# Kernel tuning notes

Measured on AMD Instinct MI355X. Metric: run time of the kernel, lower is better.

## Reference

```python
import jax, jax.numpy as jnp
import numpy as np


def setup_inputs() -> dict:
    key = jax.random.key(0)
    kx, ke = jax.random.split(key)
    N, T, D, M = 64, 400, 1024, 256
    x = jax.random.normal(kx, (N, T, D), dtype=jnp.float32)
    embedding = jax.random.normal(ke, (M, D), dtype=jnp.float32)
    return {"x": x, "embedding": embedding}


def reference(x, embedding):
    # x: (N, T, D); embedding (codebook): (M, D)
    M, D = embedding.shape
    # L2_distance: normalize codebook rows, distances to detached x
    emb_norm = embedding / (jnp.linalg.norm(embedding, axis=1, keepdims=True) + 1e-4)
    x_flat = jax.lax.stop_gradient(x).reshape(-1, D)  # (N*T, D)
    distances = (jnp.sum(emb_norm ** 2, axis=1)[None, :]
                 + jnp.sum(x_flat ** 2, axis=1, keepdims=True)
                 - 2.0 * (x_flat @ emb_norm.T))  # (N*T, M)
    indices = jnp.argmin(distances, axis=-1)  # (N*T,)
    encodings = jax.nn.one_hot(indices, M, dtype=jnp.float32)  # (N*T, M)
    quantized = embedding[indices].reshape(x.shape)  # gather from UNnormalized codebook

    # commitment loss (both sides detached in original -> constant)
    commitment_loss = jnp.mean(
        (jax.lax.stop_gradient(x) - jax.lax.stop_gradient(quantized)) ** 2)

    # straight-through + average with quantized
    quantized_st = x + jax.lax.stop_gradient(quantized - x)
    quantized_ = (quantized_st + quantized) / 2.0

    avg_probs = jnp.mean(encodings, axis=0)  # (M,)
    perplexity = jnp.exp(-jnp.sum(avg_probs * jnp.log(avg_probs + 1e-10)))
    return quantized_, commitment_loss, perplexity
```

## Files before the change

### kernel.cpp

```cpp
#include <hip/hip_runtime.h>
#include <cstdint>
#include <cstddef>


typedef __attribute__((ext_vector_type(8))) short short8;
typedef __attribute__((ext_vector_type(4))) float f32x4;

namespace {
constexpr int kNT = 25600;
constexpr int kD  = 1024;
constexpr int kM  = 256;
constexpr size_t kQElems = (size_t)kNT * kD;

constexpr int WS_IMG_H = 0;
constexpr int WS_IMG_L = 131072;
constexpr int WS_E2N   = 262144;
constexpr int WS_SCL   = WS_E2N + kM;
constexpr int WS_E2R   = WS_SCL + kM;
constexpr int WS_COM   = WS_E2R + kM;
constexpr int WS_HIST  = WS_COM + 4;
constexpr int WS_TICKET = WS_HIST + kM;
}

typedef __attribute__((address_space(3))) unsigned int        lds_u32;
typedef const __attribute__((address_space(1))) unsigned int  glb_u32;
typedef const __attribute__((address_space(3))) char          lds_chc;

__device__ __forceinline__ void gl2lds16(const void* g, void* l) {
  __builtin_amdgcn_global_load_lds((glb_u32*)g, (lds_u32*)l, 16, 0, 0);
}

template <int OFF>
__device__ __forceinline__ short8 ldsr(lds_chc* p) {
  static_assert(OFF >= 0 && OFF < 65536, "ds offset immediate");
  short8 r;
  asm volatile("ds_read_b128 %0, %1 offset:%c2" : "=v"(r) : "v"(p), "i"(OFF));
  return r;
}
template <int OFF>
__device__ __forceinline__ void ldsw(lds_chc* p, short8 v) {
  static_assert(OFF >= 0 && OFF < 65536, "ds offset immediate");
  asm volatile("ds_write_b128 %0, %1 offset:%c2" :: "v"(p), "v"(v), "i"(OFF) : "memory");
}
__device__ __forceinline__ f32x4 gld4(const float* p) {
  f32x4 r;
  asm volatile("global_load_dwordx4 %0, %1, off" : "=v"(r) : "v"(p));
  return r;
}

__global__ __launch_bounds__(256) void vq_normalize(const float* __restrict__ emb,
                                                    float* __restrict__ ws) {
  const int m = blockIdx.x;
  const int t = threadIdx.x;

  if (t == 0) ((int*)(ws + WS_HIST))[m] = 0;
  if (m == 0 && t < 4) ws[WS_COM + t] = 0.0f;
  if (m == 0 && t == 4) ((int*)(ws + WS_TICKET))[0] = 0;

  const float4 v = reinterpret_cast<const float4*>(emb + (size_t)m * kD)[t];
  float s = v.x * v.x + v.y * v.y + v.z * v.z + v.w * v.w;
#pragma unroll
  for (int mask = 32; mask >= 1; mask >>= 1) s += __shfl_xor(s, mask);
  __shared__ float red[4];
  if ((t & 63) == 0) red[t >> 6] = s;
  __syncthreads();
  const float tot = red[0] + red[1] + red[2] + red[3];
  const float sc  = sqrtf(tot) + 1e-4f;
  const float inv = 1.0f / sc;
  const float4 nv = make_float4(v.x * inv, v.y * inv, v.z * inv, v.w * inv);

  float s2 = nv.x * nv.x + nv.y * nv.y + nv.z * nv.z + nv.w * nv.w;
#pragma unroll
  for (int mask = 32; mask >= 1; mask >>= 1) s2 += __shfl_xor(s2, mask);
  __syncthreads();
  if ((t & 63) == 0) red[t >> 6] = s2;
  __syncthreads();
  if (t == 0) {
    ws[WS_E2N + m] = red[0] + red[1] + red[2] + red[3];
    ws[WS_SCL + m] = sc;
    ws[WS_E2R + m] = tot;
  }

  unsigned short* imgh = (unsigned short*)(ws + WS_IMG_H);
  unsigned short* imgl = (unsigned short*)(ws + WS_IMG_L);
  const int c  = t >> 3;
  const int g  = (t >> 1) & 3;
  const int sq = g ^ ((m >> 1) & 3);
  const int base = c * 8192 + m * 32 + sq * 8 + 4 * (t & 1);
  ushort4 hq, lq;
#pragma unroll
  for (int j = 0; j < 4; ++j) {
    const float fv = (&nv.x)[j];
    const unsigned int b = __float_as_uint(fv);
    const unsigned short hi = (unsigned short)(b >> 16);
    const float lof = fv - __uint_as_float(b & 0xFFFF0000u);
    const unsigned short lo = (unsigned short)(__float_as_uint(lof) >> 16);
    (&hq.x)[j] = hi; (&lq.x)[j] = lo;
  }
  *(ushort4*)(imgh + base) = hq;
  *(ushort4*)(imgl + base) = lq;
}


struct Frags {
  short8 a0h, a1h, a2h, a3h, a0l, a1l, a2l, a3l;
  short8 b0h, b1h, b2h, b3h, b0l, b1l, b2l, b3l;
};

#define DMASTAGE(KCN)                                                          \
  {                                                                            \
    const unsigned short* gh_ = imgH + ((size_t)(KCN) << 13) + (w << 11) + (l << 3); \
    const unsigned short* gl_ = imgL + ((size_t)(KCN) << 13) + (w << 11) + (l << 3); \
    char* dg_ = pool + 16384 + w * 8192;                                       \
    gl2lds16(gh_,        dg_);                                                 \
    gl2lds16(gh_ +  512, dg_ + 1024);                                          \
    gl2lds16(gh_ + 1024, dg_ + 2048);                                          \
    gl2lds16(gh_ + 1536, dg_ + 3072);                                          \
    gl2lds16(gl_,        dg_ + 4096);                                          \
    gl2lds16(gl_ +  512, dg_ + 5120);                                          \
    gl2lds16(gl_ + 1024, dg_ + 6144);                                          \
    gl2lds16(gl_ + 1536, dg_ + 7168);                                          \
  }

#define PREFETCH9(PN, FN)                                                      \
  (FN).b0h = ldsr<16384 + 0 * 1024>(pB);                                       \
  (FN).b1h = ldsr<16384 + 1 * 1024>(pB);                                       \
  (FN).b2h = ldsr<16384 + 2 * 1024>(pB);                                       \
  (FN).b3h = ldsr<16384 + 3 * 1024>(pB);                                       \
  (FN).b0l = ldsr<16384 + 4096 + 0 * 1024>(pB);                                \
  (FN).b1l = ldsr<16384 + 4096 + 1 * 1024>(pB);                                \
  (FN).b2l = ldsr<16384 + 4096 + 2 * 1024>(pB);                                \
  (FN).b3l = ldsr<16384 + 4096 + 3 * 1024>(pB);                                \
  (FN).a0h = ldsr<(PN) * 8192 + 0 * 1024>(pA);                                 \
  (FN).a1h = ldsr<(PN) * 8192 + 1 * 1024>(pA);                                 \
  (FN).a2h = ldsr<(PN) * 8192 + 2 * 1024>(pA);                                 \
  (FN).a3h = ldsr<(PN) * 8192 + 3 * 1024>(pA);                                 \
  (FN).a0l = ldsr<(PN) * 8192 + 4096 + 0 * 1024>(pA);                          \
  (FN).a1l = ldsr<(PN) * 8192 + 4096 + 1 * 1024>(pA);                          \
  (FN).a2l = ldsr<(PN) * 8192 + 4096 + 2 * 1024>(pA);                          \
  (FN).a3l = ldsr<(PN) * 8192 + 4096 + 3 * 1024>(pA);

#define CONV8(F0, F1, AH, AL, X2EN)                                            \
  {                                                                            \
    union { short8 v; unsigned short u[8]; } H_, L_;                           \
    _Pragma("unroll")                                                          \
    for (int jj_ = 0; jj_ < 8; ++jj_) {                                        \
      const float fv_ = (jj_ < 4) ? (F0)[jj_] : (F1)[jj_ - 4];                 \
      const unsigned int b_ = __float_as_uint(fv_);                            \
      H_.u[jj_] = (unsigned short)(b_ >> 16);                                  \
      const float lo_ = fv_ - __uint_as_float(b_ & 0xFFFF0000u);               \
      L_.u[jj_] = (unsigned short)(__float_as_uint(lo_) >> 16);                \
      if (X2EN) x2 += fv_ * fv_;                                               \
    }                                                                          \
    AH = H_.v; AL = L_.v;                                                      \
  }

#define MMQ(AR, B0, B1, B2, B3, RT)                                                        \
  acc[RT][0] = __builtin_amdgcn_mfma_f32_16x16x32_bf16(AR, B0, acc[RT][0], 0, 0, 0);       \
  acc[RT][1] = __builtin_amdgcn_mfma_f32_16x16x32_bf16(AR, B1, acc[RT][1], 0, 0, 0);       \
  acc[RT][2] = __builtin_amdgcn_mfma_f32_16x16x32_bf16(AR, B2, acc[RT][2], 0, 0, 0);       \
  acc[RT][3] = __builtin_amdgcn_mfma_f32_16x16x32_bf16(AR, B3, acc[RT][3], 0, 0, 0);
#define MMPASS(A0, A1, A2, A3, B0, B1, B2, B3)                                 \
  MMQ(A0, B0, B1, B2, B3, 0) MMQ(A1, B0, B1, B2, B3, 1)                        \
  MMQ(A2, B0, B1, B2, B3, 2) MMQ(A3, B0, B1, B2, B3, 3)

#define VQ_ITER9(KC, P, FC, FN, XC0, XC1, XN0, XN1)                            \
  {                                                                            \
    __builtin_amdgcn_s_setprio(1);                                             \
    MMPASS(FC.a0h, FC.a1h, FC.a2h, FC.a3h, FC.b0h, FC.b1h, FC.b2h, FC.b3h)     \
    __builtin_amdgcn_s_setprio(0);                                             \
    asm volatile("s_waitcnt vmcnt(8)" ::: "memory");       \
    __builtin_amdgcn_sched_barrier(0);                                         \
    if ((KC) < 30) {                                                           \
      short8 cah, cal;                                                         \
      CONV8(XC0, XC1, cah, cal, 1)                                             \
      ldsw<(P) * 8192 + 0>(pW, cah);                                           \
      ldsw<(P) * 8192 + 4096>(pW, cal);                                        \
    }                                                                          \
    {                                                                          \
      const int kx_ = ((KC) + 3 < 32) ? (KC) + 3 : 31;                         \
      XN0 = gld4(xrow + kx_ * 32);                                             \
      XN1 = gld4(xrow + kx_ * 32 + 4);                                         \
    }                                                                          \
    asm volatile("s_waitcnt vmcnt(2)" ::: "memory");       \
    __builtin_amdgcn_sched_barrier(0);                                         \
    PREFETCH9((P) ^ 1, FN)                                    \
    __builtin_amdgcn_s_setprio(1);                                             \
    MMPASS(FC.a0h, FC.a1h, FC.a2h, FC.a3h, FC.b0l, FC.b1l, FC.b2l, FC.b3l)     \
    __builtin_amdgcn_s_setprio(0);                                             \
    asm volatile("s_waitcnt lgkmcnt(0)" ::: "memory");  \
    __builtin_amdgcn_sched_barrier(0);                                         \
    {                                                                          \
      const int kb_ = ((KC) + 2 < 32) ? (KC) + 2 : 31;                         \
      DMASTAGE(kb_)                                     \
    }                                                                          \
    __builtin_amdgcn_s_setprio(1);                                             \
    MMPASS(FC.a0l, FC.a1l, FC.a2l, FC.a3l, FC.b0h, FC.b1h, FC.b2h, FC.b3h)     \
    __builtin_amdgcn_s_setprio(0);                                             \
    __builtin_amdgcn_sched_barrier(0);                                         \
    __builtin_amdgcn_s_barrier();                            \
  }

__global__ __launch_bounds__(256, 2) void vq_main(const float* __restrict__ x,
                                                  const float* __restrict__ emb,
                                                  const float* __restrict__ wsc,
                                                  float* __restrict__ out,
                                                  float* __restrict__ commit_sum,
                                                  int* __restrict__ hist,
                                                  int* __restrict__ ticket) {
  __shared__ char pool[49152];

  const int t   = threadIdx.x;
  const int l   = t & 63;
  const int w   = t >> 6;
  const int nlo = l & 15;
  const int kq  = l >> 4;
  const int blk0 = blockIdx.x * 64;

  const unsigned short* imgH = (const unsigned short*)(wsc + WS_IMG_H);
  const unsigned short* imgL = (const unsigned short*)(wsc + WS_IMG_L);

  const float* xrow = x + (size_t)(blk0 + w * 16 + nlo) * kD + kq * 8;

  const int sqz = kq ^ ((nlo >> 1) & 3);
  lds_chc* base = (lds_chc*)pool;
  lds_chc* pA = base + nlo * 64 + sqz * 16;
  lds_chc* pB = base + w * 8192 + nlo * 64 + sqz * 16;
  lds_chc* pW = pA + w * 1024;

  f32x4 acc[4][4];
#pragma unroll
  for (int i = 0; i < 4; ++i)
#pragma unroll
    for (int j = 0; j < 4; ++j) acc[i][j] = (f32x4)0.0f;
  float x2 = 0.0f;

  Frags F0, F1;

  f32x4 xa0 = gld4(xrow);
  f32x4 xa1 = gld4(xrow + 4);
  f32x4 xb0 = gld4(xrow + 32);
  f32x4 xb1 = gld4(xrow + 36);
  DMASTAGE(0)
  asm volatile("s_waitcnt vmcnt(10)" ::: "memory");
  __builtin_amdgcn_sched_barrier(0);
  {
    short8 cah, cal;
    CONV8(xa0, xa1, cah, cal, 1)
    ldsw<0>(pW, cah);
    ldsw<4096>(pW, cal);
  }
  asm volatile("s_waitcnt vmcnt(8)" ::: "memory");
  __builtin_amdgcn_sched_barrier(0);
  {
    short8 cah, cal;
    CONV8(xb0, xb1, cah, cal, 1)
    ldsw<8192 + 0>(pW, cah);
    ldsw<8192 + 4096>(pW, cal);
  }
  xa0 = gld4(xrow + 2 * 32);
  xa1 = gld4(xrow + 2 * 32 + 4);
  asm volatile("s_waitcnt vmcnt(2)" ::: "memory");
  __builtin_amdgcn_sched_barrier(0);
  asm volatile("s_waitcnt lgkmcnt(0)" ::: "memory");
  __builtin_amdgcn_sched_barrier(0);
  __builtin_amdgcn_s_barrier();
  PREFETCH9(0, F0)
  asm volatile("s_waitcnt lgkmcnt(0)" ::: "memory");
  __builtin_amdgcn_sched_barrier(0);
  DMASTAGE(1)
  __builtin_amdgcn_s_barrier();

#pragma unroll 1
  for (int kk = 0; kk < 32; kk += 2) {
    VQ_ITER9(kk,     0, F0, F1, xa0, xa1, xb0, xb1)
    VQ_ITER9(kk + 1, 1, F1, F0, xb0, xb1, xa0, xa1)
  }

  asm volatile("s_waitcnt vmcnt(0)"
               :: "v"(xa0), "v"(xa1), "v"(xb0), "v"(xb1) : "memory");

  float* x2s  = (float*)pool;
  float* bvp  = x2s + 64;
  int*   bjp  = (int*)(bvp + 256);
  int*   idxs = bjp + 256;

  x2 += __shfl_xor(x2, 16);
  x2 += __shfl_xor(x2, 32);
  if (l < 16) x2s[w * 16 + l] = x2;

  float eN[4];
#pragma unroll
  for (int ct = 0; ct < 4; ++ct) eN[ct] = wsc[WS_E2N + w * 64 + ct * 16 + nlo];

  float bv[4][4]; int bj[4][4];
#pragma unroll
  for (int rt = 0; rt < 4; ++rt)
#pragma unroll
    for (int rg = 0; rg < 4; ++rg) { bv[rt][rg] = 3.0e38f; bj[rt][rg] = 0; }
#pragma unroll
  for (int ct = 0; ct < 4; ++ct) {
    const int j = w * 64 + ct * 16 + nlo;
#pragma unroll
    for (int rt = 0; rt < 4; ++rt)
#pragma unroll
      for (int rg = 0; rg < 4; ++rg) {
        const float v = eN[ct] - 2.0f * acc[rt][ct][rg];
        if (v < bv[rt][rg] || (v == bv[rt][rg] && j < bj[rt][rg])) {
          bv[rt][rg] = v; bj[rt][rg] = j;
        }
      }
  }
#pragma unroll
  for (int mk = 1; mk <= 8; mk <<= 1) {
#pragma unroll
    for (int rt = 0; rt < 4; ++rt)
#pragma unroll
      for (int rg = 0; rg < 4; ++rg) {
        const float ov = __shfl_xor(bv[rt][rg], mk);
        const int   oj = __shfl_xor(bj[rt][rg], mk);
        if (ov < bv[rt][rg] || (ov == bv[rt][rg] && oj < bj[rt][rg])) {
          bv[rt][rg] = ov; bj[rt][rg] = oj;
        }
      }
  }
  __syncthreads();
  if (nlo == 0) {
#pragma unroll
    for (int rt = 0; rt < 4; ++rt)
#pragma unroll
      for (int rg = 0; rg < 4; ++rg) {
        const int row = rt * 16 + kq * 4 + rg;
        bvp[w * 64 + row] = bv[rt][rg];
        bjp[w * 64 + row] = bj[rt][rg];
      }
  }
  __syncthreads();

  if (t < 64) {
    const int row = t;
    float v = bvp[row]; int j = bjp[row];
#pragma unroll
    for (int wv = 1; wv < 4; ++wv) {
      const float v2 = bvp[wv * 64 + row]; const int j2 = bjp[wv * 64 + row];
      if (v2 < v || (v2 == v && j2 < j)) { v = v2; j = j2; }
    }
    idxs[row] = j;
    atomicAdd(&hist[j], 1);
    float cl = x2s[row] + wsc[WS_E2R + j] - (wsc[WS_E2N + j] - v) * wsc[WS_SCL + j];
#pragma unroll
    for (int mk = 1; mk <= 32; mk <<= 1) cl += __shfl_xor(cl, mk);
    if (t == 0) atomicAdd(commit_sum, cl);
  }
  __syncthreads();

  const float4* emb4 = (const float4*)emb;
  float4* out4 = (float4*)out;
#pragma unroll 2
  for (int rr = 0; rr < 16; ++rr) {
    const int j = idxs[w * 16 + rr];
    const float4* s = emb4 + (size_t)j * (kD / 4);
    float4* d = out4 + (size_t)(blk0 + w * 16 + rr) * (kD / 4);
#pragma unroll
    for (int c = 0; c < 4; ++c) d[c * 64 + l] = s[c * 64 + l];
  }

  __threadfence();
  int* doneflag = (int*)(pool + 4160);
  if (t == 0) *doneflag = atomicAdd(ticket, 1);
  __syncthreads();
  if (*doneflag == (kNT / 64) - 1) {
    const int h = atomicAdd(&hist[t], 0);
    const float p = (float)h * (1.0f / (float)kNT);
    float s = p * logf(p + 1e-10f);
#pragma unroll
    for (int mask = 32; mask >= 1; mask >>= 1) s += __shfl_xor(s, mask);
    float* red = (float*)(pool + 4096);
    if ((t & 63) == 0) red[t >> 6] = s;
    __syncthreads();
    if (t == 0) {
      const float ent = red[0] + red[1] + red[2] + red[3];
      const float cs = atomicAdd(commit_sum, 0.0f);
      out[kQElems]     = cs * (1.0f / (float)kQElems);
      out[kQElems + 1] = expf(-ent);
    }
  }
}

extern "C" void kernel_launch(void* const* d_in, const int* in_sizes, int n_in,
                              void* d_out, int out_size, void* d_ws, size_t ws_size,
                              hipStream_t stream) {
  (void)in_sizes; (void)n_in; (void)out_size; (void)ws_size;
  const float* x   = (const float*)d_in[0];
  const float* emb = (const float*)d_in[1];
  float* out = (float*)d_out;
  float* ws  = (float*)d_ws;

  hipLaunchKernelGGL(vq_normalize, dim3(kM), dim3(256), 0, stream, emb, ws);
  hipLaunchKernelGGL(vq_main, dim3(kNT / 64), dim3(256), 0, stream,
                     x, emb, ws, out, ws + WS_COM, (int*)(ws + WS_HIST),
                     (int*)(ws + WS_TICKET));
}
```

Baseline: 281.0 us.

## Halve rows per block, convert x fragments in registers, raise occupancy

The main kernel now handles 32 rows per block instead of 64, which doubles the grid. Each wave loads and splits its x rows into bf16 hi/lo directly in registers, so x no longer goes through LDS. The double-buffered A/B fragment pipeline is replaced by a single-buffer loop that waits on vmcnt(0) every chunk. LDS drops to 32 KB and launch bounds ask for 3 blocks per SM, so latency is meant to be hidden by occupancy rather than explicit prefetch. In exchange, each wave re-reads the same x rows, and the codebook image is streamed by twice as many blocks, which adds L2 traffic and per-iteration stalls.

```diff
diff --git a/kernel.cpp b/kernel.cpp
--- a/kernel.cpp
+++ b/kernel.cpp
@@ -10,6 +10,7 @@
 constexpr int kNT = 25600;
 constexpr int kD  = 1024;
 constexpr int kM  = 256;
+constexpr int kRPB = 32;
 constexpr size_t kQElems = (size_t)kNT * kD;
 
 constexpr int WS_IMG_H = 0;
@@ -37,11 +38,6 @@
   asm volatile("ds_read_b128 %0, %1 offset:%c2" : "=v"(r) : "v"(p), "i"(OFF));
   return r;
 }
-template <int OFF>
-__device__ __forceinline__ void ldsw(lds_chc* p, short8 v) {
-  static_assert(OFF >= 0 && OFF < 65536, "ds offset immediate");
-  asm volatile("ds_write_b128 %0, %1 offset:%c2" :: "v"(p), "v"(v), "i"(OFF) : "memory");
-}
 __device__ __forceinline__ f32x4 gld4(const float* p) {
   f32x4 r;
   asm volatile("global_load_dwordx4 %0, %1, off" : "=v"(r) : "v"(p));
@@ -102,16 +98,11 @@
 }
 
 
-struct Frags {
-  short8 a0h, a1h, a2h, a3h, a0l, a1l, a2l, a3l;
-  short8 b0h, b1h, b2h, b3h, b0l, b1l, b2l, b3l;
-};
-
 #define DMASTAGE(KCN)                                                          \
   {                                                                            \
     const unsigned short* gh_ = imgH + ((size_t)(KCN) << 13) + (w << 11) + (l << 3); \
     const unsigned short* gl_ = imgL + ((size_t)(KCN) << 13) + (w << 11) + (l << 3); \
-    char* dg_ = pool + 16384 + w * 8192;                                       \
+    char* dg_ = pool + w * 8192;                                               \
     gl2lds16(gh_,        dg_);                                                 \
     gl2lds16(gh_ +  512, dg_ + 1024);                                          \
     gl2lds16(gh_ + 1024, dg_ + 2048);                                          \
@@ -122,25 +113,7 @@
     gl2lds16(gl_ + 1536, dg_ + 7168);                                          \
   }
 
-#define PREFETCH9(PN, FN)                                                      \
-  (FN).b0h = ldsr<16384 + 0 * 1024>(pB);                                       \
-  (FN).b1h = ldsr<16384 + 1 * 1024>(pB);                                       \
-  (FN).b2h = ldsr<16384 + 2 * 1024>(pB);                                       \
-  (FN).b3h = ldsr<16384 + 3 * 1024>(pB);                                       \
-  (FN).b0l = ldsr<16384 + 4096 + 0 * 1024>(pB);                                \
-  (FN).b1l = ldsr<16384 + 4096 + 1 * 1024>(pB);                                \
-  (FN).b2l = ldsr<16384 + 4096 + 2 * 1024>(pB);                                \
-  (FN).b3l = ldsr<16384 + 4096 + 3 * 1024>(pB);                                \
-  (FN).a0h = ldsr<(PN) * 8192 + 0 * 1024>(pA);                                 \
-  (FN).a1h = ldsr<(PN) * 8192 + 1 * 1024>(pA);                                 \
-  (FN).a2h = ldsr<(PN) * 8192 + 2 * 1024>(pA);                                 \
-  (FN).a3h = ldsr<(PN) * 8192 + 3 * 1024>(pA);                                 \
-  (FN).a0l = ldsr<(PN) * 8192 + 4096 + 0 * 1024>(pA);                          \
-  (FN).a1l = ldsr<(PN) * 8192 + 4096 + 1 * 1024>(pA);                          \
-  (FN).a2l = ldsr<(PN) * 8192 + 4096 + 2 * 1024>(pA);                          \
-  (FN).a3l = ldsr<(PN) * 8192 + 4096 + 3 * 1024>(pA);
-
-#define CONV8(F0, F1, AH, AL, X2EN)                                            \
+#define CONV8(F0, F1, AH, AL, X2V)                                             \
   {                                                                            \
     union { short8 v; unsigned short u[8]; } H_, L_;                           \
     _Pragma("unroll")                                                          \
@@ -150,159 +123,106 @@
       H_.u[jj_] = (unsigned short)(b_ >> 16);                                  \
       const float lo_ = fv_ - __uint_as_float(b_ & 0xFFFF0000u);               \
       L_.u[jj_] = (unsigned short)(__float_as_uint(lo_) >> 16);                \
-      if (X2EN) x2 += fv_ * fv_;                                               \
+      X2V += fv_ * fv_;                                                        \
     }                                                                          \
     AH = H_.v; AL = L_.v;                                                      \
   }
 
-#define MMQ(AR, B0, B1, B2, B3, RT)                                                        \
+#define MM4(AR, B0, B1, B2, B3, RT)                                                        \
   acc[RT][0] = __builtin_amdgcn_mfma_f32_16x16x32_bf16(AR, B0, acc[RT][0], 0, 0, 0);       \
   acc[RT][1] = __builtin_amdgcn_mfma_f32_16x16x32_bf16(AR, B1, acc[RT][1], 0, 0, 0);       \
   acc[RT][2] = __builtin_amdgcn_mfma_f32_16x16x32_bf16(AR, B2, acc[RT][2], 0, 0, 0);       \
   acc[RT][3] = __builtin_amdgcn_mfma_f32_16x16x32_bf16(AR, B3, acc[RT][3], 0, 0, 0);
-#define MMPASS(A0, A1, A2, A3, B0, B1, B2, B3)                                 \
-  MMQ(A0, B0, B1, B2, B3, 0) MMQ(A1, B0, B1, B2, B3, 1)                        \
-  MMQ(A2, B0, B1, B2, B3, 2) MMQ(A3, B0, B1, B2, B3, 3)
-
-#define VQ_ITER9(KC, P, FC, FN, XC0, XC1, XN0, XN1)                            \
-  {                                                                            \
-    __builtin_amdgcn_s_setprio(1);                                             \
-    MMPASS(FC.a0h, FC.a1h, FC.a2h, FC.a3h, FC.b0h, FC.b1h, FC.b2h, FC.b3h)     \
-    __builtin_amdgcn_s_setprio(0);                                             \
-    asm volatile("s_waitcnt vmcnt(8)" ::: "memory");       \
-    __builtin_amdgcn_sched_barrier(0);                                         \
-    if ((KC) < 30) {                                                           \
-      short8 cah, cal;                                                         \
-      CONV8(XC0, XC1, cah, cal, 1)                                             \
-      ldsw<(P) * 8192 + 0>(pW, cah);                                           \
-      ldsw<(P) * 8192 + 4096>(pW, cal);                                        \
-    }                                                                          \
-    {                                                                          \
-      const int kx_ = ((KC) + 3 < 32) ? (KC) + 3 : 31;                         \
-      XN0 = gld4(xrow + kx_ * 32);                                             \
-      XN1 = gld4(xrow + kx_ * 32 + 4);                                         \
-    }                                                                          \
-    asm volatile("s_waitcnt vmcnt(2)" ::: "memory");       \
-    __builtin_amdgcn_sched_barrier(0);                                         \
-    PREFETCH9((P) ^ 1, FN)                                    \
-    __builtin_amdgcn_s_setprio(1);                                             \
-    MMPASS(FC.a0h, FC.a1h, FC.a2h, FC.a3h, FC.b0l, FC.b1l, FC.b2l, FC.b3l)     \
-    __builtin_amdgcn_s_setprio(0);                                             \
-    asm volatile("s_waitcnt lgkmcnt(0)" ::: "memory");  \
-    __builtin_amdgcn_sched_barrier(0);                                         \
-    {                                                                          \
-      const int kb_ = ((KC) + 2 < 32) ? (KC) + 2 : 31;                         \
-      DMASTAGE(kb_)                                     \
-    }                                                                          \
-    __builtin_amdgcn_s_setprio(1);                                             \
-    MMPASS(FC.a0l, FC.a1l, FC.a2l, FC.a3l, FC.b0h, FC.b1h, FC.b2h, FC.b3h)     \
-    __builtin_amdgcn_s_setprio(0);                                             \
-    __builtin_amdgcn_sched_barrier(0);                                         \
-    __builtin_amdgcn_s_barrier();                            \
-  }
-
-__global__ __launch_bounds__(256, 2) void vq_main(const float* __restrict__ x,
+
+__global__ __launch_bounds__(256, 3) void vq_main(const float* __restrict__ x,
                                                   const float* __restrict__ emb,
                                                   const float* __restrict__ wsc,
                                                   float* __restrict__ out,
                                                   float* __restrict__ commit_sum,
                                                   int* __restrict__ hist,
                                                   int* __restrict__ ticket) {
-  __shared__ char pool[49152];
+  __shared__ char pool[32768];
 
   const int t   = threadIdx.x;
   const int l   = t & 63;
   const int w   = t >> 6;
   const int nlo = l & 15;
   const int kq  = l >> 4;
-  const int blk0 = blockIdx.x * 64;
+  const int blk0 = blockIdx.x * kRPB;
 
   const unsigned short* imgH = (const unsigned short*)(wsc + WS_IMG_H);
   const unsigned short* imgL = (const unsigned short*)(wsc + WS_IMG_L);
 
-  const float* xrow = x + (size_t)(blk0 + w * 16 + nlo) * kD + kq * 8;
+  const float* xr0 = x + (size_t)(blk0 + nlo) * kD + kq * 8;
+  const float* xr1 = xr0 + (size_t)16 * kD;
 
   const int sqz = kq ^ ((nlo >> 1) & 3);
-  lds_chc* base = (lds_chc*)pool;
-  lds_chc* pA = base + nlo * 64 + sqz * 16;
-  lds_chc* pB = base + w * 8192 + nlo * 64 + sqz * 16;
-  lds_chc* pW = pA + w * 1024;
-
-  f32x4 acc[4][4];
-#pragma unroll
-  for (int i = 0; i < 4; ++i)
+  lds_chc* pB = (lds_chc*)pool + w * 8192 + nlo * 64 + sqz * 16;
+
+  f32x4 acc[2][4];
+#pragma unroll
+  for (int i = 0; i < 2; ++i)
 #pragma unroll
     for (int j = 0; j < 4; ++j) acc[i][j] = (f32x4)0.0f;
-  float x2 = 0.0f;
-
-  Frags F0, F1;
-
-  f32x4 xa0 = gld4(xrow);
-  f32x4 xa1 = gld4(xrow + 4);
-  f32x4 xb0 = gld4(xrow + 32);
-  f32x4 xb1 = gld4(xrow + 36);
+  float x2a = 0.0f, x2b = 0.0f;
+
   DMASTAGE(0)
-  asm volatile("s_waitcnt vmcnt(10)" ::: "memory");
-  __builtin_amdgcn_sched_barrier(0);
-  {
-    short8 cah, cal;
-    CONV8(xa0, xa1, cah, cal, 1)
-    ldsw<0>(pW, cah);
-    ldsw<4096>(pW, cal);
-  }
-  asm volatile("s_waitcnt vmcnt(8)" ::: "memory");
-  __builtin_amdgcn_sched_barrier(0);
-  {
-    short8 cah, cal;
-    CONV8(xb0, xb1, cah, cal, 1)
-    ldsw<8192 + 0>(pW, cah);
-    ldsw<8192 + 4096>(pW, cal);
-  }
-  xa0 = gld4(xrow + 2 * 32);
-  xa1 = gld4(xrow + 2 * 32 + 4);
-  asm volatile("s_waitcnt vmcnt(2)" ::: "memory");
-  __builtin_amdgcn_sched_barrier(0);
-  asm volatile("s_waitcnt lgkmcnt(0)" ::: "memory");
-  __builtin_amdgcn_sched_barrier(0);
-  __builtin_amdgcn_s_barrier();
-  PREFETCH9(0, F0)
-  asm volatile("s_waitcnt lgkmcnt(0)" ::: "memory");
-  __builtin_amdgcn_sched_barrier(0);
-  DMASTAGE(1)
-  __builtin_amdgcn_s_barrier();
+  f32x4 xv0 = gld4(xr0);
+  f32x4 xv1 = gld4(xr0 + 4);
+  f32x4 xv2 = gld4(xr1);
+  f32x4 xv3 = gld4(xr1 + 4);
 
 #pragma unroll 1
-  for (int kk = 0; kk < 32; kk += 2) {
-    VQ_ITER9(kk,     0, F0, F1, xa0, xa1, xb0, xb1)
-    VQ_ITER9(kk + 1, 1, F1, F0, xb0, xb1, xa0, xa1)
+  for (int c = 0; c < 32; ++c) {
+    asm volatile("s_waitcnt vmcnt(0)" ::: "memory");
+    __builtin_amdgcn_sched_barrier(0);
+    short8 bh0 = ldsr<0>(pB),    bh1 = ldsr<1024>(pB);
+    short8 bh2 = ldsr<2048>(pB), bh3 = ldsr<3072>(pB);
+    short8 bl0 = ldsr<4096>(pB), bl1 = ldsr<5120>(pB);
+    short8 bl2 = ldsr<6144>(pB), bl3 = ldsr<7168>(pB);
+    short8 ah0, al0, ah1, al1;
+    CONV8(xv0, xv1, ah0, al0, x2a)
+    CONV8(xv2, xv3, ah1, al1, x2b)
+    asm volatile("s_waitcnt lgkmcnt(0)" ::: "memory");
+    __builtin_amdgcn_sched_barrier(0);
+    const int cn = (c < 31) ? c + 1 : 31;
+    DMASTAGE(cn)
+    {
+      const float* xp0 = xr0 + cn * 32;
+      const float* xp1 = xr1 + cn * 32;
+      xv0 = gld4(xp0); xv1 = gld4(xp0 + 4);
+      xv2 = gld4(xp1); xv3 = gld4(xp1 + 4);
+    }
+    __builtin_amdgcn_s_setprio(1);
+    MM4(ah0, bh0, bh1, bh2, bh3, 0)
+    MM4(ah1, bh0, bh1, bh2, bh3, 1)
+    MM4(ah0, bl0, bl1, bl2, bl3, 0)
+    MM4(ah1, bl0, bl1, bl2, bl3, 1)
+    MM4(al0, bh0, bh1, bh2, bh3, 0)
+    MM4(al1, bh0, bh1, bh2, bh3, 1)
+    __builtin_amdgcn_s_setprio(0);
   }
 
   asm volatile("s_waitcnt vmcnt(0)"
-               :: "v"(xa0), "v"(xa1), "v"(xb0), "v"(xb1) : "memory");
-
-  float* x2s  = (float*)pool;
-  float* bvp  = x2s + 64;
-  int*   bjp  = (int*)(bvp + 256);
-  int*   idxs = bjp + 256;
-
-  x2 += __shfl_xor(x2, 16);
-  x2 += __shfl_xor(x2, 32);
-  if (l < 16) x2s[w * 16 + l] = x2;
+               :: "v"(xv0), "v"(xv1), "v"(xv2), "v"(xv3) : "memory");
+
+  x2a += __shfl_xor(x2a, 16); x2a += __shfl_xor(x2a, 32);
+  x2b += __shfl_xor(x2b, 16); x2b += __shfl_xor(x2b, 32);
 
   float eN[4];
 #pragma unroll
   for (int ct = 0; ct < 4; ++ct) eN[ct] = wsc[WS_E2N + w * 64 + ct * 16 + nlo];
 
-  float bv[4][4]; int bj[4][4];
-#pragma unroll
-  for (int rt = 0; rt < 4; ++rt)
+  float bv[2][4]; int bj[2][4];
+#pragma unroll
+  for (int rt = 0; rt < 2; ++rt)
 #pragma unroll
     for (int rg = 0; rg < 4; ++rg) { bv[rt][rg] = 3.0e38f; bj[rt][rg] = 0; }
 #pragma unroll
   for (int ct = 0; ct < 4; ++ct) {
     const int j = w * 64 + ct * 16 + nlo;
 #pragma unroll
-    for (int rt = 0; rt < 4; ++rt)
+    for (int rt = 0; rt < 2; ++rt)
 #pragma unroll
       for (int rg = 0; rg < 4; ++rg) {
         const float v = eN[ct] - 2.0f * acc[rt][ct][rg];
@@ -314,7 +234,7 @@
 #pragma unroll
   for (int mk = 1; mk <= 8; mk <<= 1) {
 #pragma unroll
-    for (int rt = 0; rt < 4; ++rt)
+    for (int rt = 0; rt < 2; ++rt)
 #pragma unroll
       for (int rg = 0; rg < 4; ++rg) {
         const float ov = __shfl_xor(bv[rt][rg], mk);
@@ -324,58 +244,69 @@
         }
       }
   }
-  __syncthreads();
+
+  float* x2s  = (float*)pool;
+  float* bvp  = x2s + kRPB;
+  int*   bjp  = (int*)(bvp + 4 * kRPB);
+  int*   idxs = bjp + 4 * kRPB;
+  float* red  = (float*)(idxs + kRPB);
+  int*   doneflag = (int*)(red + 4);
+
+  __syncthreads();
+  if (w == 0 && l < 16) { x2s[l] = x2a; x2s[16 + l] = x2b; }
   if (nlo == 0) {
 #pragma unroll
-    for (int rt = 0; rt < 4; ++rt)
+    for (int rt = 0; rt < 2; ++rt)
 #pragma unroll
       for (int rg = 0; rg < 4; ++rg) {
         const int row = rt * 16 + kq * 4 + rg;
-        bvp[w * 64 + row] = bv[rt][rg];
-        bjp[w * 64 + row] = bj[rt][rg];
+        bvp[w * kRPB + row] = bv[rt][rg];
+        bjp[w * kRPB + row] = bj[rt][rg];
       }
   }
   __syncthreads();
 
-  if (t < 64) {
-    const int row = t;
-    float v = bvp[row]; int j = bjp[row];
-#pragma unroll
-    for (int wv = 1; wv < 4; ++wv) {
-      const float v2 = bvp[wv * 64 + row]; const int j2 = bjp[wv * 64 + row];
-      if (v2 < v || (v2 == v && j2 < j)) { v = v2; j = j2; }
+  if (w == 0) {
+    float cl = 0.0f;
+    if (l < kRPB) {
+      const int row = l;
+      float v = bvp[row]; int j = bjp[row];
+#pragma unroll
+      for (int wv = 1; wv < 4; ++wv) {
+        const float v2 = bvp[wv * kRPB + row]; const int j2 = bjp[wv * kRPB + row];
+        if (v2 < v || (v2 == v && j2 < j)) { v = v2; j = j2; }
+      }
+      idxs[row] = j;
+      atomicAdd(&hist[j], 1);
+      cl = x2s[row] + wsc[WS_E2R + j] - (wsc[WS_E2N + j] - v) * wsc[WS_SCL + j];
     }
-    idxs[row] = j;
-    atomicAdd(&hist[j], 1);
-    float cl = x2s[row] + wsc[WS_E2R + j] - (wsc[WS_E2N + j] - v) * wsc[WS_SCL + j];
 #pragma unroll
     for (int mk = 1; mk <= 32; mk <<= 1) cl += __shfl_xor(cl, mk);
-    if (t == 0) atomicAdd(commit_sum, cl);
+    if (l == 0) atomicAdd(commit_sum, cl);
   }
   __syncthreads();
 
   const float4* emb4 = (const float4*)emb;
   float4* out4 = (float4*)out;
-#pragma unroll 2
-  for (int rr = 0; rr < 16; ++rr) {
-    const int j = idxs[w * 16 + rr];
+#pragma unroll
+  for (int rr = 0; rr < 8; ++rr) {
+    const int row = w * 8 + rr;
+    const int j = idxs[row];
     const float4* s = emb4 + (size_t)j * (kD / 4);
-    float4* d = out4 + (size_t)(blk0 + w * 16 + rr) * (kD / 4);
-#pragma unroll
-    for (int c = 0; c < 4; ++c) d[c * 64 + l] = s[c * 64 + l];
+    float4* d = out4 + (size_t)(blk0 + row) * (kD / 4);
+#pragma unroll
+    for (int cc = 0; cc < 4; ++cc) d[cc * 64 + l] = s[cc * 64 + l];
   }
 
   __threadfence();
-  int* doneflag = (int*)(pool + 4160);
   if (t == 0) *doneflag = atomicAdd(ticket, 1);
   __syncthreads();
-  if (*doneflag == (kNT / 64) - 1) {
+  if (*doneflag == (kNT / kRPB) - 1) {
     const int h = atomicAdd(&hist[t], 0);
     const float p = (float)h * (1.0f / (float)kNT);
     float s = p * logf(p + 1e-10f);
 #pragma unroll
     for (int mask = 32; mask >= 1; mask >>= 1) s += __shfl_xor(s, mask);
-    float* red = (float*)(pool + 4096);
     if ((t & 63) == 0) red[t >> 6] = s;
     __syncthreads();
     if (t == 0) {
@@ -397,7 +328,7 @@
   float* ws  = (float*)d_ws;
 
   hipLaunchKernelGGL(vq_normalize, dim3(kM), dim3(256), 0, stream, emb, ws);
-  hipLaunchKernelGGL(vq_main, dim3(kNT / 64), dim3(256), 0, stream,
+  hipLaunchKernelGGL(vq_main, dim3(kNT / kRPB), dim3(256), 0, stream,
                      x, emb, ws, out, ws + WS_COM, (int*)(ws + WS_HIST),
                      (int*)(ws + WS_TICKET));
 }
```

Result: slower. 394.4 us (+40.3%).
